# Kernel tuning notes

Hardware: AMD Instinct MI355X
Metric: run time of the kernel (lower is better)

Reference implementation:

```python
import jax, jax.numpy as jnp
import numpy as np

# Dimensions matching init_kwargs
B, S, D, d_feat, O = 64, 1024, 64, 2, 10
L = S // 2  # label_site
STD = 0.01  # 'random_eye' init noise scale


def setup_inputs() -> dict:
    key = jax.random.key(0)
    k1, k2, k3, k4 = jax.random.split(key, 4)
    x = jax.random.normal(k1, (B, S, d_feat), dtype=jnp.float32)
    # InputRegion tensors, bond_str 'slri': eye over (l, r) broadcast over (s, i)
    W_left = jnp.eye(D, dtype=jnp.float32)[None, :, :, None] \
        + STD * jax.random.normal(k2, (L, D, D, d_feat), dtype=jnp.float32)
    W_right = jnp.eye(D, dtype=jnp.float32)[None, :, :, None] \
        + STD * jax.random.normal(k3, (S - L, D, D, d_feat), dtype=jnp.float32)
    # OutputSite tensor, bond_str 'olr': eye over (l, r) broadcast over o
    out_core = jnp.eye(D, dtype=jnp.float32)[None, :, :] \
        + STD * jax.random.normal(k4, (O, D, D), dtype=jnp.float32)
    return {"x": x, "W_left": W_left, "out_core": out_core, "W_right": W_right}


def reference(x, W_left, out_core, W_right):
    # x: [B, S, d]; W_left: [L, D, D, d]; out_core: [O, D, D]; W_right: [S-L, D, D, d]
    Ls = W_left.shape[0]
    Dv = W_left.shape[1]
    Bv = x.shape[0]
    # Per-site matrices (einsum 'slri,bsi->bslr'), laid out scan-major [S, B, D, D]
    mats_l = jnp.einsum('slri,bsi->sblr', W_left, x[:, :Ls])
    mats_r = jnp.einsum('slri,bsi->sblr', W_right, x[:, Ls:])
    # Open boundary edge vectors e = [1, 0, ..., 0]
    e = jnp.zeros((Dv,), dtype=x.dtype).at[0].set(1.0)
    v0 = jnp.broadcast_to(e, (Bv, Dv))
    # Left-to-right vector propagation through left chain
    def lstep(v, m):
        return jnp.einsum('bl,blr->br', v, m), None
    vL, _ = jax.lax.scan(lstep, v0, mats_l)
    # Right-to-left vector propagation through right chain
    def rstep(w, m):
        return jnp.einsum('blr,br->bl', m, w), None
    wR, _ = jax.lax.scan(rstep, v0, mats_r, reverse=True)
    # Contract through the output core: [B, O]
    return jnp.einsum('bl,olr,br->bo', vL, out_core, wR)
```

## Files before the change

kernel.cpp:

```cpp
#include <hip/hip_runtime.h>
#include <stdint.h>

#define NSITE 512
#define DD    64
#define NB    64
#define NO    10
#define NSEG  16
#define SEGLEN 32
#define SLAB_BYTES 32768
#define PACK_BYTES 16384

typedef short bf16x8 __attribute__((ext_vector_type(8)));
typedef float f32x16 __attribute__((ext_vector_type(16)));

__device__ __forceinline__ uint32_t pk2(float a, float b) {
    return __builtin_amdgcn_perm(__float_as_uint(b), __float_as_uint(a), 0x07060302);
}

__global__ __launch_bounds__(256) void pack_kernel(float* __restrict__ wl,
                                                   float* __restrict__ wr) {
    const int g = blockIdx.x;
    const int right = (g >= NSITE) ? 1 : 0;
    const int s = right ? g - NSITE : g;
    float* base = (right ? wr : wl) + (size_t)s * (SLAB_BYTES / 4);

    __shared__ float2 st[DD * 65];
    const float2* src2 = (const float2*)base;
    for (int e = threadIdx.x; e < DD * DD; e += 256)
        st[(e >> 6) * 65 + (e & 63)] = src2[e];
    __syncthreads();

    uint32_t* out = (uint32_t*)base;
    #pragma unroll
    for (int rr = 0; rr < 16; ++rr) {
        const int od = rr * 256 + threadIdx.x;
        const int chunk = od >> 8, i = chunk >> 3, sk = chunk & 7;
        const int H = (od >> 7) & 1, m5 = (od >> 2) & 31, d = od & 3;
        const int m = 32 * i + m5, k = 8 * sk + 4 * H + d;
        const float2 a = right ? st[m * 65 + k] : st[k * 65 + m];
        out[od] = pk2(a.x, a.y);
    }
}

__device__ __forceinline__ void dma16(const void* gp, void* lp) {
    __builtin_amdgcn_global_load_lds(
        (const __attribute__((address_space(1))) uint32_t*)gp,
        (__attribute__((address_space(3))) uint32_t*)lp, 16, 0, 0);
}

__global__ __launch_bounds__(256, 2) void stage1_kernel(
        const float* __restrict__ x, float* __restrict__ wl, float* __restrict__ wr) {
    const int bid  = blockIdx.x;
    const int side = bid >> 8;
    const int seg  = (bid >> 4) & 15;
    const int bq   = bid & 15;
    const int wave = threadIdx.x >> 6;
    const int lane = threadIdx.x & 63;
    const int b    = bq * 4 + wave;
    const int m5   = lane & 31;
    const int H    = lane >> 5;

    __shared__ __align__(16) char ring[4][PACK_BYTES];
    __shared__ float2 xs[4][SEGLEN];

    char* wbuf = (char*)(side ? wr : wl);

    if (lane < SEGLEN) {
        const float2* xp = ((const float2*)x) + (size_t)b * 1024 + (side ? NSITE : 0);
        const int sg = seg * SEGLEN + (side ? SEGLEN - 1 - lane : lane);
        xs[wave][lane] = xp[sg];
    }

    auto siteAddr = [&](int t) -> const char* {
        const int sg = seg * SEGLEN + (side ? SEGLEN - 1 - t : t);
        return wbuf + (size_t)sg * SLAB_BYTES;
    };

    #pragma unroll
    for (int t0 = 0; t0 < 3; ++t0) {
        const char* sb = siteAddr(t0);
        #pragma unroll
        for (int c = 0; c < 4; ++c) {
            const int ch = wave * 4 + c;
            dma16(sb + ch * 1024 + lane * 16, ring[t0] + ch * 1024);
        }
    }

    f32x16 accP[2][2], accQ[2][2];
    #pragma unroll
    for (int i = 0; i < 2; ++i)
        #pragma unroll
        for (int j = 0; j < 2; ++j)
            #pragma unroll
            for (int q = 0; q < 16; ++q) {
                const int row = (q & 3) + 8 * (q >> 2) + 4 * H;
                accP[i][j][q] = (i == j && row == m5) ? 1.f : 0.f;
            }

    auto body = [&](int t, f32x16 (&tin)[2][2], f32x16 (&tout)[2][2]) {
        int t3 = t + 3; if (t3 > SEGLEN - 1) t3 = SEGLEN - 1;
        {
            const char* sb = siteAddr(t3);
            char* lb = ring[(t + 3) & 3];
            #pragma unroll
            for (int c = 0; c < 4; ++c) {
                const int ch = wave * 4 + c;
                dma16(sb + ch * 1024 + lane * 16, lb + ch * 1024);
            }
        }
        asm volatile("s_waitcnt vmcnt(12)" ::: "memory");
        asm volatile("s_barrier" ::: "memory");

        const char* rb = ring[t & 3];
        uint4 af[2][8];
        #pragma unroll
        for (int i = 0; i < 2; ++i)
            #pragma unroll
            for (int sk = 0; sk < 8; ++sk)
                af[i][sk] = *(const uint4*)(rb + (i * 8 + sk) * 1024 + lane * 16);

        const float2 xv = xs[wave][t];
        float2 x01; x01.x = xv.x; x01.y = xv.y;

        #pragma unroll
        for (int i = 0; i < 2; ++i)
            #pragma unroll
            for (int j = 0; j < 2; ++j)
                tout[i][j] = 0;

        #pragma unroll
        for (int sk = 0; sk < 8; ++sk) {
            const int mi = sk >> 2, qb = 4 * (sk & 3);
            union { bf16x8 v; uint32_t u[4]; } bf[2];
            #pragma unroll
            for (int j = 0; j < 2; ++j) {
                #pragma unroll
                for (int e = 0; e < 2; ++e) {
                    float2 vp;
                    vp.x = tin[mi][j][qb + 2 * e];
                    vp.y = tin[mi][j][qb + 2 * e + 1];
                    float2 d0, d1;
                    asm("v_pk_mul_f32 %0, %1, %2 op_sel:[0,0] op_sel_hi:[1,0]"
                        : "=v"(d0) : "v"(x01), "v"(vp));
                    asm("v_pk_mul_f32 %0, %1, %2 op_sel:[0,1] op_sel_hi:[1,1]"
                        : "=v"(d1) : "v"(x01), "v"(vp));
                    bf[j].u[2 * e]     = pk2(d0.x, d0.y);
                    bf[j].u[2 * e + 1] = pk2(d1.x, d1.y);
                }
            }
            #pragma unroll
            for (int i = 0; i < 2; ++i) {
                union { bf16x8 v; uint4 u; } a; a.u = af[i][sk];
                #pragma unroll
                for (int j = 0; j < 2; ++j)
                    tout[i][j] = __builtin_amdgcn_mfma_f32_32x32x16_bf16(
                        a.v, bf[j].v, tout[i][j], 0, 0, 0);
            }
        }
    };

    for (int t = 0; t < SEGLEN; t += 2) {
        body(t,     accP, accQ);
        body(t + 1, accQ, accP);
    }

    {
        const int p = b * NSEG + seg;
        char* pdst = wbuf + (size_t)(p >> 1) * SLAB_BYTES + PACK_BYTES + (p & 1) * 8192;
        #pragma unroll
        for (int i = 0; i < 2; ++i)
            #pragma unroll
            for (int j = 0; j < 2; ++j) {
                const int c = 32 * j + m5;
                #pragma unroll
                for (int Q = 0; Q < 4; ++Q) {
                    const int r0 = 32 * i + 8 * Q + 4 * H;
                    uint2 val;
                    val.x = pk2(accP[i][j][4 * Q + 0], accP[i][j][4 * Q + 1]);
                    val.y = pk2(accP[i][j][4 * Q + 2], accP[i][j][4 * Q + 3]);
                    *(uint2*)(pdst + c * 128 + r0 * 2) = val;
                }
            }
    }
    asm volatile("s_waitcnt vmcnt(0)" ::: "memory");
}

__global__ __launch_bounds__(256) void tail_kernel(
        const float* __restrict__ wl, const float* __restrict__ wr,
        const float* __restrict__ core, float* __restrict__ out) {
    const int b    = blockIdx.x;
    const int tid  = threadIdx.x;
    const int side = tid >> 7;
    const int half = (tid >> 6) & 1;
    const int r    = tid & 63;

    __shared__ float vs[2][DD];
    __shared__ float part[2][2][DD];
    if (half == 0) vs[side][r] = (r == 0) ? 1.f : 0.f;
    __syncthreads();

    const char* wb = (const char*)(side ? wr : wl);
    for (int gi = 0; gi < NSEG; ++gi) {
        const int g = side ? (NSEG - 1 - gi) : gi;
        const int p = b * NSEG + g;
        const uint16_t* P = (const uint16_t*)(wb
            + (size_t)(p >> 1) * SLAB_BYTES + PACK_BYTES + (p & 1) * 8192);
        float acc = 0.f;
        #pragma unroll
        for (int cc = 0; cc < 32; ++cc) {
            const int c = half * 32 + cc;
            acc = fmaf(vs[side][c],
                       __uint_as_float(((uint32_t)P[c * 64 + r]) << 16), acc);
        }
        part[side][half][r] = acc;
        __syncthreads();
        if (half == 0) vs[side][r] = part[side][0][r] + part[side][1][r];
        __syncthreads();
    }

    const int og   = tid >> 6;
    const int lane = tid & 63;
    for (int o = og; o < NO; o += 4) {
        float a = 0.f;
        #pragma unroll 8
        for (int l = 0; l < DD; ++l)
            a += vs[0][l] * core[(o * DD + l) * DD + lane];
        a *= vs[1][lane];
        #pragma unroll
        for (int off = 32; off > 0; off >>= 1)
            a += __shfl_xor(a, off, 64);
        if (lane == 0) out[b * NO + o] = a;
    }
}

extern "C" void kernel_launch(void* const* d_in, const int* in_sizes, int n_in,
                              void* d_out, int out_size, void* d_ws, size_t ws_size,
                              hipStream_t stream) {
    const float* x    = (const float*)d_in[0];
    float*       wl   = (float*)d_in[1];
    const float* core = (const float*)d_in[2];
    float*       wr   = (float*)d_in[3];

    pack_kernel<<<2 * NSITE, 256, 0, stream>>>(wl, wr);
    stage1_kernel<<<512, 256, 0, stream>>>(x, wl, wr);
    tail_kernel<<<NB, 256, 0, stream>>>(wl, wr, core, (float*)d_out);
}
```

Measured before the change: 198.1 us.

## Process two batch rows per wave in stage1 to reuse each loaded site slab

Each wave now carries chain products for two batch elements, so every weight slab loaded into LDS feeds twice as many MFMAs. The grid halves to 256 blocks, and the prefetch ring deepens from 4 to 8 slots with a lookahead of 4 sites. The aim is to halve global and LDS traffic for weights per unit of work. The cost is roughly doubled accumulator registers and fewer resident blocks, with occupancy dropped to 1 block per CU, which may reduce latency hiding.

```diff
diff --git a/kernel.cpp b/kernel.cpp
--- a/kernel.cpp
+++ b/kernel.cpp
@@ -48,27 +48,30 @@
         (__attribute__((address_space(3))) uint32_t*)lp, 16, 0, 0);
 }
 
-__global__ __launch_bounds__(256, 2) void stage1_kernel(
+__global__ __launch_bounds__(256, 1) void stage1_kernel(
         const float* __restrict__ x, float* __restrict__ wl, float* __restrict__ wr) {
     const int bid  = blockIdx.x;
-    const int side = bid >> 8;
-    const int seg  = (bid >> 4) & 15;
-    const int bq   = bid & 15;
+    const int side = bid >> 7;
+    const int rem  = bid & 127;
+    const int seg  = rem >> 3;
+    const int bq   = rem & 7;
     const int wave = threadIdx.x >> 6;
     const int lane = threadIdx.x & 63;
-    const int b    = bq * 4 + wave;
+    const int pi   = bq * 4 + wave;
     const int m5   = lane & 31;
     const int H    = lane >> 5;
 
-    __shared__ __align__(16) char ring[4][PACK_BYTES];
-    __shared__ float2 xs[4][SEGLEN];
+    __shared__ __align__(16) char ring[8][PACK_BYTES];
+    __shared__ float2 xs[4][2][SEGLEN];
 
     char* wbuf = (char*)(side ? wr : wl);
 
-    if (lane < SEGLEN) {
-        const float2* xp = ((const float2*)x) + (size_t)b * 1024 + (side ? NSITE : 0);
-        const int sg = seg * SEGLEN + (side ? SEGLEN - 1 - lane : lane);
-        xs[wave][lane] = xp[sg];
+    {
+        const int bb = lane >> 5, tt = lane & 31;
+        const float2* xp = ((const float2*)x) + (size_t)(2 * pi + bb) * 1024
+                         + (side ? NSITE : 0);
+        const int sg = seg * SEGLEN + (side ? SEGLEN - 1 - tt : tt);
+        xs[wave][bb][tt] = xp[sg];
     }
 
     auto siteAddr = [&](int t) -> const char* {
@@ -77,7 +80,7 @@
     };
 
     #pragma unroll
-    for (int t0 = 0; t0 < 3; ++t0) {
+    for (int t0 = 0; t0 < 4; ++t0) {
         const char* sb = siteAddr(t0);
         #pragma unroll
         for (int c = 0; c < 4; ++c) {
@@ -86,32 +89,34 @@
         }
     }
 
-    f32x16 accP[2][2], accQ[2][2];
-    #pragma unroll
-    for (int i = 0; i < 2; ++i)
-        #pragma unroll
-        for (int j = 0; j < 2; ++j)
-            #pragma unroll
-            for (int q = 0; q < 16; ++q) {
-                const int row = (q & 3) + 8 * (q >> 2) + 4 * H;
-                accP[i][j][q] = (i == j && row == m5) ? 1.f : 0.f;
-            }
-
-    auto body = [&](int t, f32x16 (&tin)[2][2], f32x16 (&tout)[2][2]) {
-        int t3 = t + 3; if (t3 > SEGLEN - 1) t3 = SEGLEN - 1;
+    f32x16 sP[2][2][2], sQ[2][2][2];
+    #pragma unroll
+    for (int bb = 0; bb < 2; ++bb)
+        #pragma unroll
+        for (int i = 0; i < 2; ++i)
+            #pragma unroll
+            for (int j = 0; j < 2; ++j)
+                #pragma unroll
+                for (int q = 0; q < 16; ++q) {
+                    const int row = (q & 3) + 8 * (q >> 2) + 4 * H;
+                    sP[bb][i][j][q] = (i == j && row == m5) ? 1.f : 0.f;
+                }
+
+    auto body = [&](int t, f32x16 (&tin)[2][2][2], f32x16 (&tout)[2][2][2]) {
+        int t4 = t + 4; if (t4 > SEGLEN - 1) t4 = SEGLEN - 1;
         {
-            const char* sb = siteAddr(t3);
-            char* lb = ring[(t + 3) & 3];
+            const char* sb = siteAddr(t4);
+            char* lb = ring[(t + 4) & 7];
             #pragma unroll
             for (int c = 0; c < 4; ++c) {
                 const int ch = wave * 4 + c;
                 dma16(sb + ch * 1024 + lane * 16, lb + ch * 1024);
             }
         }
-        asm volatile("s_waitcnt vmcnt(12)" ::: "memory");
+        asm volatile("s_waitcnt vmcnt(16)" ::: "memory");
         asm volatile("s_barrier" ::: "memory");
 
-        const char* rb = ring[t & 3];
+        const char* rb = ring[t & 7];
         uint4 af[2][8];
         #pragma unroll
         for (int i = 0; i < 2; ++i)
@@ -119,53 +124,61 @@
             for (int sk = 0; sk < 8; ++sk)
                 af[i][sk] = *(const uint4*)(rb + (i * 8 + sk) * 1024 + lane * 16);
 
-        const float2 xv = xs[wave][t];
-        float2 x01; x01.x = xv.x; x01.y = xv.y;
-
-        #pragma unroll
-        for (int i = 0; i < 2; ++i)
-            #pragma unroll
-            for (int j = 0; j < 2; ++j)
-                tout[i][j] = 0;
+        const float2 xA = xs[wave][0][t];
+        const float2 xB = xs[wave][1][t];
+
+        #pragma unroll
+        for (int bb = 0; bb < 2; ++bb)
+            #pragma unroll
+            for (int i = 0; i < 2; ++i)
+                #pragma unroll
+                for (int j = 0; j < 2; ++j)
+                    tout[bb][i][j] = 0;
 
         #pragma unroll
         for (int sk = 0; sk < 8; ++sk) {
             const int mi = sk >> 2, qb = 4 * (sk & 3);
-            union { bf16x8 v; uint32_t u[4]; } bf[2];
-            #pragma unroll
-            for (int j = 0; j < 2; ++j) {
-                #pragma unroll
-                for (int e = 0; e < 2; ++e) {
-                    float2 vp;
-                    vp.x = tin[mi][j][qb + 2 * e];
-                    vp.y = tin[mi][j][qb + 2 * e + 1];
-                    float2 d0, d1;
-                    asm("v_pk_mul_f32 %0, %1, %2 op_sel:[0,0] op_sel_hi:[1,0]"
-                        : "=v"(d0) : "v"(x01), "v"(vp));
-                    asm("v_pk_mul_f32 %0, %1, %2 op_sel:[0,1] op_sel_hi:[1,1]"
-                        : "=v"(d1) : "v"(x01), "v"(vp));
-                    bf[j].u[2 * e]     = pk2(d0.x, d0.y);
-                    bf[j].u[2 * e + 1] = pk2(d1.x, d1.y);
-                }
+            union { bf16x8 v; uint32_t u[4]; } bf[2][2];
+            #pragma unroll
+            for (int bb = 0; bb < 2; ++bb) {
+                const float2 x01 = bb ? xB : xA;
+                #pragma unroll
+                for (int j = 0; j < 2; ++j)
+                    #pragma unroll
+                    for (int e = 0; e < 2; ++e) {
+                        float2 vp;
+                        vp.x = tin[bb][mi][j][qb + 2 * e];
+                        vp.y = tin[bb][mi][j][qb + 2 * e + 1];
+                        float2 d0, d1;
+                        asm("v_pk_mul_f32 %0, %1, %2 op_sel:[0,0] op_sel_hi:[1,0]"
+                            : "=v"(d0) : "v"(x01), "v"(vp));
+                        asm("v_pk_mul_f32 %0, %1, %2 op_sel:[0,1] op_sel_hi:[1,1]"
+                            : "=v"(d1) : "v"(x01), "v"(vp));
+                        bf[bb][j].u[2 * e]     = pk2(d0.x, d0.y);
+                        bf[bb][j].u[2 * e + 1] = pk2(d1.x, d1.y);
+                    }
             }
             #pragma unroll
             for (int i = 0; i < 2; ++i) {
                 union { bf16x8 v; uint4 u; } a; a.u = af[i][sk];
                 #pragma unroll
-                for (int j = 0; j < 2; ++j)
-                    tout[i][j] = __builtin_amdgcn_mfma_f32_32x32x16_bf16(
-                        a.v, bf[j].v, tout[i][j], 0, 0, 0);
+                for (int bb = 0; bb < 2; ++bb)
+                    #pragma unroll
+                    for (int j = 0; j < 2; ++j)
+                        tout[bb][i][j] = __builtin_amdgcn_mfma_f32_32x32x16_bf16(
+                            a.v, bf[bb][j].v, tout[bb][i][j], 0, 0, 0);
             }
         }
     };
 
     for (int t = 0; t < SEGLEN; t += 2) {
-        body(t,     accP, accQ);
-        body(t + 1, accQ, accP);
-    }
-
-    {
-        const int p = b * NSEG + seg;
+        body(t,     sP, sQ);
+        body(t + 1, sQ, sP);
+    }
+
+    #pragma unroll
+    for (int bb = 0; bb < 2; ++bb) {
+        const int p = (2 * pi + bb) * NSEG + seg;
         char* pdst = wbuf + (size_t)(p >> 1) * SLAB_BYTES + PACK_BYTES + (p & 1) * 8192;
         #pragma unroll
         for (int i = 0; i < 2; ++i)
@@ -176,8 +189,8 @@
                 for (int Q = 0; Q < 4; ++Q) {
                     const int r0 = 32 * i + 8 * Q + 4 * H;
                     uint2 val;
-                    val.x = pk2(accP[i][j][4 * Q + 0], accP[i][j][4 * Q + 1]);
-                    val.y = pk2(accP[i][j][4 * Q + 2], accP[i][j][4 * Q + 3]);
+                    val.x = pk2(sP[bb][i][j][4 * Q + 0], sP[bb][i][j][4 * Q + 1]);
+                    val.y = pk2(sP[bb][i][j][4 * Q + 2], sP[bb][i][j][4 * Q + 3]);
                     *(uint2*)(pdst + c * 128 + r0 * 2) = val;
                 }
             }
@@ -242,6 +255,6 @@
     float*       wr   = (float*)d_in[3];
 
     pack_kernel<<<2 * NSITE, 256, 0, stream>>>(wl, wr);
-    stage1_kernel<<<512, 256, 0, stream>>>(x, wl, wr);
+    stage1_kernel<<<256, 256, 0, stream>>>(x, wl, wr);
     tail_kernel<<<NB, 256, 0, stream>>>(wl, wr, core, (float*)d_out);
 }
```

Result: slower. 211.2 us (+6.6%).

## Give each wave a private site buffer and drop block-level barriers in stage1

Applied to the files above, without the earlier changes.

Work is remapped so each wave owns an independent (side, seg, batch) chain with its own 16KB LDS buffer. This replaces the shared 4-deep ring, which needed s_barrier every step. The next site's DMA is issued after the A fragments are read into registers and overlaps with the MFMA chain. The idea is to remove cross-wave barrier stalls, but there is now only single-buffer prefetch per wave, and every wave loads the full site slab itself, so global traffic per block rises fourfold.

```diff
diff --git a/kernel.cpp b/kernel.cpp
--- a/kernel.cpp
+++ b/kernel.cpp
@@ -50,20 +50,20 @@
 
 __global__ __launch_bounds__(256, 2) void stage1_kernel(
         const float* __restrict__ x, float* __restrict__ wl, float* __restrict__ wr) {
-    const int bid  = blockIdx.x;
-    const int side = bid >> 8;
-    const int seg  = (bid >> 4) & 15;
-    const int bq   = bid & 15;
     const int wave = threadIdx.x >> 6;
     const int lane = threadIdx.x & 63;
-    const int b    = bq * 4 + wave;
+    const int p    = blockIdx.x * 4 + wave;
+    const int side = p >> 10;
+    const int seg  = (p >> 6) & 15;
+    const int b    = p & 63;
     const int m5   = lane & 31;
     const int H    = lane >> 5;
 
-    __shared__ __align__(16) char ring[4][PACK_BYTES];
+    __shared__ __align__(16) char bufs[4][PACK_BYTES];
     __shared__ float2 xs[4][SEGLEN];
 
     char* wbuf = (char*)(side ? wr : wl);
+    char* buf  = bufs[wave];
 
     if (lane < SEGLEN) {
         const float2* xp = ((const float2*)x) + (size_t)b * 1024 + (side ? NSITE : 0);
@@ -76,17 +76,18 @@
         return wbuf + (size_t)sg * SLAB_BYTES;
     };
 
+    {
+        const char* sb = siteAddr(0);
+        #pragma unroll
+        for (int c = 0; c < 16; ++c)
+            dma16(sb + c * 1024 + lane * 16, buf + c * 1024);
+    }
+
+    f32x16 zc;
     #pragma unroll
-    for (int t0 = 0; t0 < 3; ++t0) {
-        const char* sb = siteAddr(t0);
-        #pragma unroll
-        for (int c = 0; c < 4; ++c) {
-            const int ch = wave * 4 + c;
-            dma16(sb + ch * 1024 + lane * 16, ring[t0] + ch * 1024);
-        }
-    }
-
-    f32x16 accP[2][2], accQ[2][2];
+    for (int q = 0; q < 16; ++q) zc[q] = 0.f;
+
+    f32x16 sP[2][2], sQ[2][2];
     #pragma unroll
     for (int i = 0; i < 2; ++i)
         #pragma unroll
@@ -94,46 +95,28 @@
             #pragma unroll
             for (int q = 0; q < 16; ++q) {
                 const int row = (q & 3) + 8 * (q >> 2) + 4 * H;
-                accP[i][j][q] = (i == j && row == m5) ? 1.f : 0.f;
+                sP[i][j][q] = (i == j && row == m5) ? 1.f : 0.f;
             }
 
     auto body = [&](int t, f32x16 (&tin)[2][2], f32x16 (&tout)[2][2]) {
-        int t3 = t + 3; if (t3 > SEGLEN - 1) t3 = SEGLEN - 1;
-        {
-            const char* sb = siteAddr(t3);
-            char* lb = ring[(t + 3) & 3];
-            #pragma unroll
-            for (int c = 0; c < 4; ++c) {
-                const int ch = wave * 4 + c;
-                dma16(sb + ch * 1024 + lane * 16, lb + ch * 1024);
-            }
-        }
-        asm volatile("s_waitcnt vmcnt(12)" ::: "memory");
-        asm volatile("s_barrier" ::: "memory");
-
-        const char* rb = ring[t & 3];
+        asm volatile("s_waitcnt vmcnt(0)" ::: "memory");
+
         uint4 af[2][8];
         #pragma unroll
         for (int i = 0; i < 2; ++i)
             #pragma unroll
             for (int sk = 0; sk < 8; ++sk)
-                af[i][sk] = *(const uint4*)(rb + (i * 8 + sk) * 1024 + lane * 16);
+                af[i][sk] = *(const uint4*)(buf + (i * 8 + sk) * 1024 + lane * 16);
 
         const float2 xv = xs[wave][t];
         float2 x01; x01.x = xv.x; x01.y = xv.y;
 
-        #pragma unroll
-        for (int i = 0; i < 2; ++i)
-            #pragma unroll
-            for (int j = 0; j < 2; ++j)
-                tout[i][j] = 0;
-
+        union { bf16x8 v; uint32_t u[4]; } bf[8][2];
         #pragma unroll
         for (int sk = 0; sk < 8; ++sk) {
             const int mi = sk >> 2, qb = 4 * (sk & 3);
-            union { bf16x8 v; uint32_t u[4]; } bf[2];
-            #pragma unroll
-            for (int j = 0; j < 2; ++j) {
+            #pragma unroll
+            for (int j = 0; j < 2; ++j)
                 #pragma unroll
                 for (int e = 0; e < 2; ++e) {
                     float2 vp;
@@ -144,29 +127,39 @@
                         : "=v"(d0) : "v"(x01), "v"(vp));
                     asm("v_pk_mul_f32 %0, %1, %2 op_sel:[0,1] op_sel_hi:[1,1]"
                         : "=v"(d1) : "v"(x01), "v"(vp));
-                    bf[j].u[2 * e]     = pk2(d0.x, d0.y);
-                    bf[j].u[2 * e + 1] = pk2(d1.x, d1.y);
+                    bf[sk][j].u[2 * e]     = pk2(d0.x, d0.y);
+                    bf[sk][j].u[2 * e + 1] = pk2(d1.x, d1.y);
                 }
-            }
+        }
+
+        asm volatile("s_waitcnt lgkmcnt(0)" ::: "memory");
+        if (t + 1 < SEGLEN) {
+            const char* sb = siteAddr(t + 1);
+            #pragma unroll
+            for (int c = 0; c < 16; ++c)
+                dma16(sb + c * 1024 + lane * 16, buf + c * 1024);
+        }
+
+        #pragma unroll
+        for (int sk = 0; sk < 8; ++sk)
             #pragma unroll
             for (int i = 0; i < 2; ++i) {
                 union { bf16x8 v; uint4 u; } a; a.u = af[i][sk];
                 #pragma unroll
                 for (int j = 0; j < 2; ++j)
                     tout[i][j] = __builtin_amdgcn_mfma_f32_32x32x16_bf16(
-                        a.v, bf[j].v, tout[i][j], 0, 0, 0);
+                        a.v, bf[sk][j].v, sk == 0 ? zc : tout[i][j], 0, 0, 0);
             }
-        }
     };
 
     for (int t = 0; t < SEGLEN; t += 2) {
-        body(t,     accP, accQ);
-        body(t + 1, accQ, accP);
+        body(t,     sP, sQ);
+        body(t + 1, sQ, sP);
     }
 
     {
-        const int p = b * NSEG + seg;
-        char* pdst = wbuf + (size_t)(p >> 1) * SLAB_BYTES + PACK_BYTES + (p & 1) * 8192;
+        const int pp = b * NSEG + seg;
+        char* pdst = wbuf + (size_t)(pp >> 1) * SLAB_BYTES + PACK_BYTES + (pp & 1) * 8192;
         #pragma unroll
         for (int i = 0; i < 2; ++i)
             #pragma unroll
@@ -176,8 +169,8 @@
                 for (int Q = 0; Q < 4; ++Q) {
                     const int r0 = 32 * i + 8 * Q + 4 * H;
                     uint2 val;
-                    val.x = pk2(accP[i][j][4 * Q + 0], accP[i][j][4 * Q + 1]);
-                    val.y = pk2(accP[i][j][4 * Q + 2], accP[i][j][4 * Q + 3]);
+                    val.x = pk2(sP[i][j][4 * Q + 0], sP[i][j][4 * Q + 1]);
+                    val.y = pk2(sP[i][j][4 * Q + 2], sP[i][j][4 * Q + 3]);
                     *(uint2*)(pdst + c * 128 + r0 * 2) = val;
                 }
             }
```

Measured after the change: 210.4 us. 6.2% more time.

## Split stage1 column halves across twice as many waves per block

Applied to the files above, without the earlier changes.

Stage1 blocks now run 512 threads. Each pair of waves shares one batch element, and each wave propagates only its own 32-column half of the running product. This works because the columns evolve independently. It halves the serial MFMA chain per wave, and fewer column halves per wave let the ping-pong accumulators collapse into a single in-place set. The prefetch depth and per-wave DMA chunk count shrink to match the doubled wave count, and the launch bound of 512 threads with 4 blocks per CU tightens the register budget, which risks spills.

```diff
diff --git a/kernel.cpp b/kernel.cpp
--- a/kernel.cpp
+++ b/kernel.cpp
@@ -48,15 +48,17 @@
         (__attribute__((address_space(3))) uint32_t*)lp, 16, 0, 0);
 }
 
-__global__ __launch_bounds__(256, 2) void stage1_kernel(
+__global__ __launch_bounds__(512, 4) void stage1_kernel(
         const float* __restrict__ x, float* __restrict__ wl, float* __restrict__ wr) {
     const int bid  = blockIdx.x;
     const int side = bid >> 8;
     const int seg  = (bid >> 4) & 15;
-    const int bq   = bid & 15;
+    const int bg   = bid & 15;
     const int wave = threadIdx.x >> 6;
     const int lane = threadIdx.x & 63;
-    const int b    = bq * 4 + wave;
+    const int prod = wave >> 1;
+    const int jh   = wave & 1;
+    const int b    = bg * 4 + prod;
     const int m5   = lane & 31;
     const int H    = lane >> 5;
 
@@ -65,10 +67,10 @@
 
     char* wbuf = (char*)(side ? wr : wl);
 
-    if (lane < SEGLEN) {
+    if (jh == 0 && lane < SEGLEN) {
         const float2* xp = ((const float2*)x) + (size_t)b * 1024 + (side ? NSITE : 0);
         const int sg = seg * SEGLEN + (side ? SEGLEN - 1 - lane : lane);
-        xs[wave][lane] = xp[sg];
+        xs[prod][lane] = xp[sg];
     }
 
     auto siteAddr = [&](int t) -> const char* {
@@ -77,109 +79,89 @@
     };
 
     #pragma unroll
-    for (int t0 = 0; t0 < 3; ++t0) {
+    for (int t0 = 0; t0 < 2; ++t0) {
         const char* sb = siteAddr(t0);
         #pragma unroll
-        for (int c = 0; c < 4; ++c) {
-            const int ch = wave * 4 + c;
+        for (int c = 0; c < 2; ++c) {
+            const int ch = wave * 2 + c;
             dma16(sb + ch * 1024 + lane * 16, ring[t0] + ch * 1024);
         }
     }
 
-    f32x16 accP[2][2], accQ[2][2];
+    f32x16 zc;
+    #pragma unroll
+    for (int q = 0; q < 16; ++q) zc[q] = 0.f;
+
+    f32x16 acc[2];
     #pragma unroll
     for (int i = 0; i < 2; ++i)
         #pragma unroll
-        for (int j = 0; j < 2; ++j)
-            #pragma unroll
-            for (int q = 0; q < 16; ++q) {
-                const int row = (q & 3) + 8 * (q >> 2) + 4 * H;
-                accP[i][j][q] = (i == j && row == m5) ? 1.f : 0.f;
-            }
-
-    auto body = [&](int t, f32x16 (&tin)[2][2], f32x16 (&tout)[2][2]) {
-        int t3 = t + 3; if (t3 > SEGLEN - 1) t3 = SEGLEN - 1;
+        for (int q = 0; q < 16; ++q) {
+            const int rr = (q & 3) + 8 * (q >> 2) + 4 * H;
+            acc[i][q] = (i == jh && rr == m5) ? 1.f : 0.f;
+        }
+
+    for (int t = 0; t < SEGLEN; ++t) {
+        int t2 = t + 2; if (t2 > SEGLEN - 1) t2 = SEGLEN - 1;
         {
-            const char* sb = siteAddr(t3);
-            char* lb = ring[(t + 3) & 3];
-            #pragma unroll
-            for (int c = 0; c < 4; ++c) {
-                const int ch = wave * 4 + c;
+            const char* sb = siteAddr(t2);
+            char* lb = ring[(t + 2) & 3];
+            #pragma unroll
+            for (int c = 0; c < 2; ++c) {
+                const int ch = wave * 2 + c;
                 dma16(sb + ch * 1024 + lane * 16, lb + ch * 1024);
             }
         }
-        asm volatile("s_waitcnt vmcnt(12)" ::: "memory");
+        asm volatile("s_waitcnt vmcnt(4)" ::: "memory");
         asm volatile("s_barrier" ::: "memory");
 
         const char* rb = ring[t & 3];
-        uint4 af[2][8];
-        #pragma unroll
-        for (int i = 0; i < 2; ++i)
-            #pragma unroll
-            for (int sk = 0; sk < 8; ++sk)
-                af[i][sk] = *(const uint4*)(rb + (i * 8 + sk) * 1024 + lane * 16);
-
-        const float2 xv = xs[wave][t];
+        const float2 xv = xs[prod][t];
         float2 x01; x01.x = xv.x; x01.y = xv.y;
 
-        #pragma unroll
-        for (int i = 0; i < 2; ++i)
-            #pragma unroll
-            for (int j = 0; j < 2; ++j)
-                tout[i][j] = 0;
-
+        union { bf16x8 v; uint32_t u[4]; } bf[8];
         #pragma unroll
         for (int sk = 0; sk < 8; ++sk) {
             const int mi = sk >> 2, qb = 4 * (sk & 3);
-            union { bf16x8 v; uint32_t u[4]; } bf[2];
-            #pragma unroll
-            for (int j = 0; j < 2; ++j) {
-                #pragma unroll
-                for (int e = 0; e < 2; ++e) {
-                    float2 vp;
-                    vp.x = tin[mi][j][qb + 2 * e];
-                    vp.y = tin[mi][j][qb + 2 * e + 1];
-                    float2 d0, d1;
-                    asm("v_pk_mul_f32 %0, %1, %2 op_sel:[0,0] op_sel_hi:[1,0]"
-                        : "=v"(d0) : "v"(x01), "v"(vp));
-                    asm("v_pk_mul_f32 %0, %1, %2 op_sel:[0,1] op_sel_hi:[1,1]"
-                        : "=v"(d1) : "v"(x01), "v"(vp));
-                    bf[j].u[2 * e]     = pk2(d0.x, d0.y);
-                    bf[j].u[2 * e + 1] = pk2(d1.x, d1.y);
-                }
-            }
+            #pragma unroll
+            for (int e = 0; e < 2; ++e) {
+                float2 vp;
+                vp.x = acc[mi][qb + 2 * e];
+                vp.y = acc[mi][qb + 2 * e + 1];
+                float2 d0, d1;
+                asm("v_pk_mul_f32 %0, %1, %2 op_sel:[0,0] op_sel_hi:[1,0]"
+                    : "=v"(d0) : "v"(x01), "v"(vp));
+                asm("v_pk_mul_f32 %0, %1, %2 op_sel:[0,1] op_sel_hi:[1,1]"
+                    : "=v"(d1) : "v"(x01), "v"(vp));
+                bf[sk].u[2 * e]     = pk2(d0.x, d0.y);
+                bf[sk].u[2 * e + 1] = pk2(d1.x, d1.y);
+            }
+        }
+
+        #pragma unroll
+        for (int sk = 0; sk < 8; ++sk)
             #pragma unroll
             for (int i = 0; i < 2; ++i) {
-                union { bf16x8 v; uint4 u; } a; a.u = af[i][sk];
-                #pragma unroll
-                for (int j = 0; j < 2; ++j)
-                    tout[i][j] = __builtin_amdgcn_mfma_f32_32x32x16_bf16(
-                        a.v, bf[j].v, tout[i][j], 0, 0, 0);
-            }
-        }
-    };
-
-    for (int t = 0; t < SEGLEN; t += 2) {
-        body(t,     accP, accQ);
-        body(t + 1, accQ, accP);
+                union { bf16x8 v; uint4 u; } a;
+                a.u = *(const uint4*)(rb + (i * 8 + sk) * 1024 + lane * 16);
+                acc[i] = __builtin_amdgcn_mfma_f32_32x32x16_bf16(
+                    a.v, bf[sk].v, sk == 0 ? zc : acc[i], 0, 0, 0);
+            }
     }
 
     {
-        const int p = b * NSEG + seg;
-        char* pdst = wbuf + (size_t)(p >> 1) * SLAB_BYTES + PACK_BYTES + (p & 1) * 8192;
+        const int pp = b * NSEG + seg;
+        char* pdst = wbuf + (size_t)(pp >> 1) * SLAB_BYTES + PACK_BYTES + (pp & 1) * 8192;
+        const int c = 32 * jh + m5;
         #pragma unroll
         for (int i = 0; i < 2; ++i)
             #pragma unroll
-            for (int j = 0; j < 2; ++j) {
-                const int c = 32 * j + m5;
-                #pragma unroll
-                for (int Q = 0; Q < 4; ++Q) {
-                    const int r0 = 32 * i + 8 * Q + 4 * H;
-                    uint2 val;
-                    val.x = pk2(accP[i][j][4 * Q + 0], accP[i][j][4 * Q + 1]);
-                    val.y = pk2(accP[i][j][4 * Q + 2], accP[i][j][4 * Q + 3]);
-                    *(uint2*)(pdst + c * 128 + r0 * 2) = val;
-                }
+            for (int Q = 0; Q < 4; ++Q) {
+                const int r0 = 32 * i + 8 * Q + 4 * H;
+                uint2 val;
+                val.x = pk2(acc[i][4 * Q + 0], acc[i][4 * Q + 1]);
+                val.y = pk2(acc[i][4 * Q + 2], acc[i][4 * Q + 3]);
+                *(uint2*)(pdst + c * 128 + r0 * 2) = val;
             }
     }
     asm volatile("s_waitcnt vmcnt(0)" ::: "memory");
@@ -242,6 +224,6 @@
     float*       wr   = (float*)d_in[3];
 
     pack_kernel<<<2 * NSITE, 256, 0, stream>>>(wl, wr);
-    stage1_kernel<<<512, 256, 0, stream>>>(x, wl, wr);
+    stage1_kernel<<<512, 512, 0, stream>>>(x, wl, wr);
     tail_kernel<<<NB, 256, 0, stream>>>(wl, wr, core, (float*)d_out);
 }
```

Result: faster. 193.9 us (-2.1%).
